# Kernel optimization log

Measured on AMD Instinct MI355X. Metric: run time of the kernel, lower is better.

## Reference

```python
import jax, jax.numpy as jnp
import numpy as np

B = 65536
IN = 64
H = 16
PF = 64


def _linear_params(key, out_dim, in_dim):
    k1, k2 = jax.random.split(key)
    bound = 1.0 / np.sqrt(in_dim)
    W = jax.random.uniform(k1, (out_dim, in_dim), jnp.float32, -bound, bound)
    b = jax.random.uniform(k2, (out_dim,), jnp.float32, -bound, bound)
    return W, b


def setup_inputs() -> dict:
    key = jax.random.key(0)
    ks = jax.random.split(key, 20)
    inp = {}
    for i, name in enumerate(['a', 'v', 'l', 'p_a', 'p_v', 'p_l', 'mean']):
        inp[name] = jax.random.normal(ks[i], (B, IN), jnp.float32)
    inp['Wa'], inp['ba'] = _linear_params(ks[7], H, IN)
    inp['Wv'], inp['bv'] = _linear_params(ks[8], H, IN)
    inp['Wl'], inp['bl'] = _linear_params(ks[9], H, IN)
    inp['Wap'], inp['bap'] = _linear_params(ks[10], H, IN)
    inp['Wvp'], inp['bvp'] = _linear_params(ks[11], H, IN)
    inp['Wlp'], inp['blp'] = _linear_params(ks[12], H, IN)
    inp['Wf1'], inp['bf1'] = _linear_params(ks[13], PF, H ** 3 // 16)
    inp['Wfp1'], inp['bfp1'] = _linear_params(ks[14], PF, H ** 3 // 16)
    inp['Wng'], inp['bng'] = _linear_params(ks[15], 64, 128)
    inp['rm1'] = jnp.zeros((128,), jnp.float32)  # normGate2 running_mean buffers (eval mode)
    inp['rm2'] = jnp.zeros((128,), jnp.float32)
    return inp


def _maxpool2(x):
    # 2x2 stride-2 max pool over the last two dims of [B, Hd, Wd]
    b, hd, wd = x.shape
    return x.reshape(b, hd // 2, 2, wd // 2, 2).max(axis=(2, 4))


def _trimodal_fusion(x_h, y_h, z_h):
    # outer product [B,H,H] -> pool -> [B,H*H//4,1] bmm [B,1,H] -> pool -> flatten
    f = x_h[:, :, None] * y_h[:, None, :]            # [B,16,16]
    f = _maxpool2(f)                                 # [B,8,8]
    f = f.reshape(-1, H * H // 4, 1) * z_h[:, None, :]  # [B,64,16]
    f = _maxpool2(f)                                 # [B,32,8]
    return f.reshape(x_h.shape[0], -1)               # [B,256]


def _norm_gate(x, running_mean):
    # eval-mode normGate2: y = x * sigmoid(|x - running_mean|)
    return x * jax.nn.sigmoid(jnp.abs(x - running_mean))


def reference(a, v, l, p_a, p_v, p_l, mean,
              Wa, ba, Wv, bv, Wl, bl, Wap, bap, Wvp, bvp, Wlp, blp,
              Wf1, bf1, Wfp1, bfp1, Wng, bng, rm1, rm2):
    a_h = jax.nn.sigmoid(a @ Wa.T + ba)
    v_h = jax.nn.sigmoid(v @ Wv.T + bv)
    l_h = jax.nn.sigmoid(l @ Wl.T + bl)
    fusion_1 = jax.nn.leaky_relu(_trimodal_fusion(a_h, v_h, l_h) @ Wf1.T + bf1)

    pa_h = jax.nn.sigmoid(p_a @ Wap.T + bap)
    pv_h = jax.nn.sigmoid(p_v @ Wvp.T + bvp)
    pl_h = jax.nn.sigmoid(p_l @ Wlp.T + blp)
    fusion_2 = jax.nn.leaky_relu(_trimodal_fusion(pa_h, pv_h, pl_h) @ Wfp1.T + bfp1)

    out = _norm_gate(jnp.concatenate([fusion_2, mean], axis=1), rm1)   # [B,128]
    out = out @ Wng.T + bng                                            # [B,64]
    out = _norm_gate(jnp.concatenate([out, fusion_1], axis=1), rm2)    # [B,128]
    return out
```

## Files before the change

kernel.cpp:

```cpp
#include <hip/hip_runtime.h>
#include <hip/hip_bf16.h>


typedef __attribute__((ext_vector_type(8))) short short8;
typedef __attribute__((ext_vector_type(4))) float f32x4;

#define MFMA16(A, B, C) __builtin_amdgcn_mfma_f32_16x16x32_bf16((A), (B), (C), 0, 0, 0)

__device__ __forceinline__ float fast_sigmoid(float x) {
    return __builtin_amdgcn_rcpf(1.0f + __expf(-x));
}
__device__ __forceinline__ float gate(float x, float rm) {
    return x * fast_sigmoid(fabsf(x - rm));
}
__device__ __forceinline__ float lrelu(float x) {
    return x >= 0.0f ? x : 0.01f * x;
}
__device__ __forceinline__ short f2bf(float f) {
    union { float f; unsigned u; } x; x.f = f;
    unsigned r = (x.u + 0x7FFF + ((x.u >> 16) & 1)) >> 16;
    return (short)r;
}
__device__ __forceinline__ short8 pack8(const float* xs) {
    union { short8 s; __hip_bfloat162 h[4]; } u;
    #pragma unroll
    for (int i = 0; i < 4; ++i) {
        float2 t; t.x = xs[2 * i]; t.y = xs[2 * i + 1];
        u.h[i] = __float22bfloat162_rn(t);
    }
    return u.s;
}
__device__ __forceinline__ f32x4 pmax_xor(f32x4 v, int mask) {
    f32x4 r;
    #pragma unroll
    for (int i = 0; i < 4; ++i) r[i] = fmaxf(v[i], __shfl_xor(v[i], mask, 64));
    return r;
}

__device__ __forceinline__ void dma_1k(const short* src, short* dst_lds, int lane) {
    __builtin_amdgcn_global_load_lds(
        (const __attribute__((address_space(1))) unsigned int*)(const void*)(src + lane * 8),
        (__attribute__((address_space(3))) unsigned int*)(void*)(dst_lds),
        16, 0, 0);
}

__device__ __forceinline__ void proj_mfma2r(const float4* in,
                                            const short8* __restrict__ wfr,
                                            const float* __restrict__ bias,
                                            int lane, f32x4& h0, f32x4& h1) {
    const int m = lane & 15;
    f32x4 a0; a0[0] = a0[1] = a0[2] = a0[3] = 0.0f;
    f32x4 a1 = a0;
    #pragma unroll
    for (int t = 0; t < 2; ++t) {
        const short8 frag = wfr[t * 64 + lane];
        float xs0[8] = {in[2*t].x, in[2*t].y, in[2*t].z, in[2*t].w,
                        in[2*t+1].x, in[2*t+1].y, in[2*t+1].z, in[2*t+1].w};
        float xs1[8] = {in[4+2*t].x, in[4+2*t].y, in[4+2*t].z, in[4+2*t].w,
                        in[4+2*t+1].x, in[4+2*t+1].y, in[4+2*t+1].z, in[4+2*t+1].w};
        a0 = MFMA16(pack8(xs0), frag, a0);
        a1 = MFMA16(pack8(xs1), frag, a1);
    }
    const float bn = bias[m];
    #pragma unroll
    for (int r = 0; r < 4; ++r) {
        h0[r] = fast_sigmoid(a0[r] + bn);
        h1[r] = fast_sigmoid(a1[r] + bn);
    }
}

__device__ __forceinline__ void stage_pools(f32x4 hx, f32x4 hy, f32x4 hz, int lane,
                                            float* __restrict__ sX,
                                            float* __restrict__ sY,
                                            float* __restrict__ sZ) {
    const int quad = lane >> 4, ln = lane & 15;
    f32x4 X = pmax_xor(hx, 1);
    f32x4 Y = pmax_xor(pmax_xor(hy, 1), 2);
    f32x4 Z = pmax_xor(hz, 1);
    #pragma unroll
    for (int r = 0; r < 4; ++r) {
        const int sm = quad * 4 + r;
        sX[(ln >> 1) * 16 + sm] = X[r];
        sY[(ln >> 2) * 16 + sm] = Y[r];
        sZ[(ln >> 1) * 16 + sm] = Z[r];
    }
}

__device__ __forceinline__ void fusion_mfma2(const short8* __restrict__ wfr,
                                             const float* __restrict__ bias,
                                             const float* __restrict__ sP0,
                                             const float* __restrict__ sP1,
                                             int lane,
                                             f32x4 acc0[4], f32x4 acc1[4]) {
    const int m = lane & 15, quad = lane >> 4;
    const float* sX0 = sP0; const float* sY0 = sP0 + 128; const float* sZ0 = sP0 + 192;
    const float* sX1 = sP1; const float* sY1 = sP1 + 128; const float* sZ1 = sP1 + 192;
    #pragma unroll
    for (int nt = 0; nt < 4; ++nt) {
        const float bb = bias[nt * 16 + m];
        acc0[nt][0] = acc0[nt][1] = acc0[nt][2] = acc0[nt][3] = bb;
        acc1[nt][0] = acc1[nt][1] = acc1[nt][2] = acc1[nt][3] = bb;
    }
    float zr0[8], zr1[8], xr0[8], xr1[8];
    #pragma unroll
    for (int j = 0; j < 8; ++j) {
        zr0[j] = sZ0[j * 16 + m]; zr1[j] = sZ1[j * 16 + m];
        xr0[j] = sX0[j * 16 + m]; xr1[j] = sX1[j * 16 + m];
    }
    const float yq0 = sY0[quad * 16 + m];
    const float yq1 = sY1[quad * 16 + m];
    #pragma unroll
    for (int t = 0; t < 8; ++t) {
        const float xy0 = xr0[t] * yq0;
        const float xy1 = xr1[t] * yq1;
        float p0[8], p1[8];
        #pragma unroll
        for (int j = 0; j < 8; ++j) { p0[j] = xy0 * zr0[j]; p1[j] = xy1 * zr1[j]; }
        const short8 af0 = pack8(p0);
        const short8 af1 = pack8(p1);
        #pragma unroll
        for (int nt = 0; nt < 4; ++nt) {
            const short8 frag = wfr[(t * 4 + nt) * 64 + lane];
            acc0[nt] = MFMA16(af0, frag, acc0[nt]);
            acc1[nt] = MFMA16(af1, frag, acc1[nt]);
        }
    }
}

__global__ __launch_bounds__(256, 2)
void fused_fwd(const float* __restrict__ a,  const float* __restrict__ v,
               const float* __restrict__ l,  const float* __restrict__ pa,
               const float* __restrict__ pv, const float* __restrict__ pl,
               const float* __restrict__ mean,
               const float* __restrict__ ba,  const float* __restrict__ bv_,
               const float* __restrict__ bl_, const float* __restrict__ bap,
               const float* __restrict__ bvp, const float* __restrict__ blp,
               const float* __restrict__ bf1, const float* __restrict__ bfp1,
               const float* __restrict__ bng,
               const float* __restrict__ rm1, const float* __restrict__ rm2,
               const short* __restrict__ ws, float* __restrict__ out) {
    __shared__ __align__(16) short sFrag[27648];
    __shared__ __align__(16) float sScr[4][1280];

    const int tid = threadIdx.x;
    const int lane = tid & 63;
    const int w = tid >> 6;
    const int m = lane & 15;
    const int quad = lane >> 4;
    const int p1 = blockIdx.x & 1;
    const int p  = blockIdx.x >> 1;

    {
        const int nU = p1 ? 38 : 54;
        for (int u = w; u < nU; u += 4) {
            const short* src;
            if (u < 6)       src = ws + (p1 ? 0 : 3072) + u * 512;
            else if (u < 38) src = ws + (p1 ? 6144 : 22528) + (u - 6) * 512;
            else             src = ws + 38912 + (u - 38) * 512;
            dma_1k(src, sFrag + u * 512, lane);
        }
    }
    __syncthreads();

    const short8* projT = (const short8*)sFrag;
    const short8* fusT  = (const short8*)(sFrag + 3072);
    const short8* ngT   = (const short8*)(sFrag + 19456);

    float* sP0 = sScr[w];
    float* sP1 = sP0 + 320;
    short* sF0 = (short*)sScr[w];
    short* sF1 = sF0 + 1280;

    for (int c = 0; c < 2; ++c) {
        const int srow0 = (p * 2 + c) * 128 + w * 32;

        if (!p1) {
            float4 inA[8], inB[8], inC[8], inM[8];
            {
                const float* x0 = pa + (size_t)srow0 * 64;
                const float* x1 = pv + (size_t)srow0 * 64;
                const float* x2 = pl + (size_t)srow0 * 64;
                #pragma unroll
                for (int i = 0; i < 8; ++i) {
                    const int tile = i >> 2, t = (i >> 1) & 1, hf = i & 1;
                    const size_t off = (size_t)(tile * 16 + m) * 64 + t * 32 + quad * 8 + hf * 4;
                    inA[i] = *(const float4*)(x0 + off);
                    inB[i] = *(const float4*)(x1 + off);
                    inC[i] = *(const float4*)(x2 + off);
                    inM[i] = *(const float4*)(mean + (size_t)(srow0 + tile * 16 + m) * 64
                                              + t * 32 + quad * 8 + hf * 4);
                }
            }

            f32x4 hx0, hx1, hy0, hy1, hz0, hz1;
            proj_mfma2r(inA, projT + 0 * 128, bap, lane, hx0, hx1);
            proj_mfma2r(inB, projT + 1 * 128, bvp, lane, hy0, hy1);
            proj_mfma2r(inC, projT + 2 * 128, blp, lane, hz0, hz1);
            stage_pools(hx0, hy0, hz0, lane, sP0, sP0 + 128, sP0 + 192);
            stage_pools(hx1, hy1, hz1, lane, sP1, sP1 + 128, sP1 + 192);

            f32x4 f20[4], f21[4];
            fusion_mfma2(fusT, bfp1, sP0, sP1, lane, f20, f21);

            #pragma unroll
            for (int nt = 0; nt < 4; ++nt) {
                const float r1 = rm1[nt * 16 + m];
                #pragma unroll
                for (int r = 0; r < 4; ++r) {
                    sF0[(quad * 4 + r) * 80 + nt * 16 + m] = f2bf(gate(lrelu(f20[nt][r]), r1));
                    sF1[(quad * 4 + r) * 80 + nt * 16 + m] = f2bf(gate(lrelu(f21[nt][r]), r1));
                }
            }

            f32x4 h0[4], h1[4];
            #pragma unroll
            for (int nt = 0; nt < 4; ++nt) {
                const float bb = bng[nt * 16 + m];
                h0[nt][0] = h0[nt][1] = h0[nt][2] = h0[nt][3] = bb;
                h1[nt][0] = h1[nt][1] = h1[nt][2] = h1[nt][3] = bb;
            }
            #pragma unroll
            for (int t = 0; t < 2; ++t) {
                const short8 af0 = *(const short8*)(sF0 + m * 80 + t * 32 + quad * 8);
                const short8 af1 = *(const short8*)(sF1 + m * 80 + t * 32 + quad * 8);
                #pragma unroll
                for (int nt = 0; nt < 4; ++nt) {
                    const short8 frag = ngT[(t * 4 + nt) * 64 + lane];
                    h0[nt] = MFMA16(af0, frag, h0[nt]);
                    h1[nt] = MFMA16(af1, frag, h1[nt]);
                }
            }
            #pragma unroll
            for (int t2 = 0; t2 < 2; ++t2) {
                const float4* rp = (const float4*)(rm1 + 64 + t2 * 32 + quad * 8);
                float4 r0 = rp[0], r1 = rp[1];
                float4 u0 = inM[2 * t2], u1 = inM[2 * t2 + 1];
                float4 w0 = inM[4 + 2 * t2], w1 = inM[4 + 2 * t2 + 1];
                float g0[8] = { gate(u0.x, r0.x), gate(u0.y, r0.y), gate(u0.z, r0.z), gate(u0.w, r0.w),
                                gate(u1.x, r1.x), gate(u1.y, r1.y), gate(u1.z, r1.z), gate(u1.w, r1.w) };
                float g1[8] = { gate(w0.x, r0.x), gate(w0.y, r0.y), gate(w0.z, r0.z), gate(w0.w, r0.w),
                                gate(w1.x, r1.x), gate(w1.y, r1.y), gate(w1.z, r1.z), gate(w1.w, r1.w) };
                const short8 af0 = pack8(g0);
                const short8 af1 = pack8(g1);
                #pragma unroll
                for (int nt = 0; nt < 4; ++nt) {
                    const short8 frag = ngT[((2 + t2) * 4 + nt) * 64 + lane];
                    h0[nt] = MFMA16(af0, frag, h0[nt]);
                    h1[nt] = MFMA16(af1, frag, h1[nt]);
                }
            }

            #pragma unroll
            for (int nt = 0; nt < 4; ++nt) {
                const float r2a = rm2[nt * 16 + m];
                #pragma unroll
                for (int r = 0; r < 4; ++r) {
                    const size_t row0 = (size_t)(srow0 + quad * 4 + r) * 128;
                    const size_t row1 = (size_t)(srow0 + 16 + quad * 4 + r) * 128;
                    out[row0 + nt * 16 + m] = gate(h0[nt][r], r2a);
                    out[row1 + nt * 16 + m] = gate(h1[nt][r], r2a);
                }
            }
        } else {
            float4 inA[8], inB[8], inC[8];
            {
                const float* x0 = a + (size_t)srow0 * 64;
                const float* x1 = v + (size_t)srow0 * 64;
                const float* x2 = l + (size_t)srow0 * 64;
                #pragma unroll
                for (int i = 0; i < 8; ++i) {
                    const int tile = i >> 2, t = (i >> 1) & 1, hf = i & 1;
                    const size_t off = (size_t)(tile * 16 + m) * 64 + t * 32 + quad * 8 + hf * 4;
                    inA[i] = *(const float4*)(x0 + off);
                    inB[i] = *(const float4*)(x1 + off);
                    inC[i] = *(const float4*)(x2 + off);
                }
            }

            f32x4 hx0, hx1, hy0, hy1, hz0, hz1;
            proj_mfma2r(inA, projT + 0 * 128, ba, lane, hx0, hx1);
            proj_mfma2r(inB, projT + 1 * 128, bv_, lane, hy0, hy1);
            proj_mfma2r(inC, projT + 2 * 128, bl_, lane, hz0, hz1);
            stage_pools(hx0, hy0, hz0, lane, sP0, sP0 + 128, sP0 + 192);
            stage_pools(hx1, hy1, hz1, lane, sP1, sP1 + 128, sP1 + 192);

            f32x4 f10[4], f11[4];
            fusion_mfma2(fusT, bf1, sP0, sP1, lane, f10, f11);

            #pragma unroll
            for (int nt = 0; nt < 4; ++nt) {
                const float r2b = rm2[64 + nt * 16 + m];
                #pragma unroll
                for (int r = 0; r < 4; ++r) {
                    const size_t row0 = (size_t)(srow0 + quad * 4 + r) * 128;
                    const size_t row1 = (size_t)(srow0 + 16 + quad * 4 + r) * 128;
                    out[row0 + 64 + nt * 16 + m] = gate(lrelu(f10[nt][r]), r2b);
                    out[row1 + 64 + nt * 16 + m] = gate(lrelu(f11[nt][r]), r2b);
                }
            }
        }
    }
}

__global__ void build_frags(const float* __restrict__ Wa,  const float* __restrict__ Wv,
                            const float* __restrict__ Wl,  const float* __restrict__ Wap,
                            const float* __restrict__ Wvp, const float* __restrict__ Wlp,
                            const float* __restrict__ Wf1, const float* __restrict__ Wfp1,
                            const float* __restrict__ Wng, short* __restrict__ ws) {
    const int i = blockIdx.x * 256 + threadIdx.x;
    if (i >= 47104) return;
    float val;
    if (i < 6144) {
        const float* W[6] = {Wa, Wv, Wl, Wap, Wvp, Wlp};
        const int mi = i >> 10, r = i & 1023;
        const int t = r >> 9, lane = (r >> 3) & 63, j = r & 7;
        val = W[mi][(lane & 15) * 64 + t * 32 + (lane >> 4) * 8 + j];
    } else if (i < 38912) {
        int r = i - 6144;
        const float* W = (r < 16384) ? Wf1 : Wfp1;
        r &= 16383;
        const int tn = r >> 9, lane = (r >> 3) & 63, j = r & 7;
        const int t = tn >> 2, nt = tn & 3;
        val = W[(nt * 16 + (lane & 15)) * 256 + t * 32 + (lane >> 4) * 8 + j];
    } else {
        const int r = i - 38912;
        const int tn = r >> 9, lane = (r >> 3) & 63, j = r & 7;
        const int t = tn >> 2, nt = tn & 3;
        val = Wng[(nt * 16 + (lane & 15)) * 128 + t * 32 + (lane >> 4) * 8 + j];
    }
    ws[i] = f2bf(val);
}

extern "C" void kernel_launch(void* const* d_in, const int* in_sizes, int n_in,
                              void* d_out, int out_size, void* d_ws, size_t ws_size,
                              hipStream_t stream) {
    const float* a    = (const float*)d_in[0];
    const float* v    = (const float*)d_in[1];
    const float* l    = (const float*)d_in[2];
    const float* pa   = (const float*)d_in[3];
    const float* pv   = (const float*)d_in[4];
    const float* pl   = (const float*)d_in[5];
    const float* mean = (const float*)d_in[6];
    const float* Wa   = (const float*)d_in[7];
    const float* ba   = (const float*)d_in[8];
    const float* Wv   = (const float*)d_in[9];
    const float* bv   = (const float*)d_in[10];
    const float* Wl   = (const float*)d_in[11];
    const float* bl   = (const float*)d_in[12];
    const float* Wap  = (const float*)d_in[13];
    const float* bap  = (const float*)d_in[14];
    const float* Wvp  = (const float*)d_in[15];
    const float* bvp  = (const float*)d_in[16];
    const float* Wlp  = (const float*)d_in[17];
    const float* blp  = (const float*)d_in[18];
    const float* Wf1  = (const float*)d_in[19];
    const float* bf1  = (const float*)d_in[20];
    const float* Wfp1 = (const float*)d_in[21];
    const float* bfp1 = (const float*)d_in[22];
    const float* Wng  = (const float*)d_in[23];
    const float* bng  = (const float*)d_in[24];
    const float* rm1  = (const float*)d_in[25];
    const float* rm2  = (const float*)d_in[26];

    short* ws = (short*)d_ws;

    build_frags<<<184, 256, 0, stream>>>(Wa, Wv, Wl, Wap, Wvp, Wlp,
                                         Wf1, Wfp1, Wng, ws);
    fused_fwd<<<512, 256, 0, stream>>>(a, v, l, pa, pv, pl, mean,
                                       ba, bv, bl, bap, bvp, blp,
                                       bf1, bfp1, bng, rm1, rm2,
                                       ws, (float*)d_out);
}
```

Before: 42.43 us.

## Issue input loads via inline asm with staged vmcnt waits; stage biases in LDS

Input loads now go through inline-asm global_load_dwordx4, grouped per tensor. Explicit s_waitcnt vmcnt(N) barriers let each projection start as soon as its own input has arrived, instead of waiting for all loads. The mean-tensor wait is pushed back to just before its use. Biases and running means are packed into the workspace by build_frags and copied into LDS alongside the weight fragments, which removes scattered global loads from the compute path. This relies on the vmcnt counts matching the issued loads exactly, and the asm volatile loads block compiler reordering.

```diff
diff --git a/kernel.cpp b/kernel.cpp
--- a/kernel.cpp
+++ b/kernel.cpp
@@ -6,6 +6,11 @@
 typedef __attribute__((ext_vector_type(4))) float f32x4;
 
 #define MFMA16(A, B, C) __builtin_amdgcn_mfma_f32_16x16x32_bf16((A), (B), (C), 0, 0, 0)
+
+#define ASM_LOAD_F4(dst, p) \
+    asm volatile("global_load_dwordx4 %0, %1, off" : "=v"(dst) : "v"(p) : "memory")
+#define VMWAIT(N) do { asm volatile("s_waitcnt vmcnt(" #N ")" ::: "memory"); \
+                       __builtin_amdgcn_sched_barrier(0); } while (0)
 
 __device__ __forceinline__ float fast_sigmoid(float x) {
     return __builtin_amdgcn_rcpf(1.0f + __expf(-x));
@@ -44,7 +49,7 @@
         16, 0, 0);
 }
 
-__device__ __forceinline__ void proj_mfma2r(const float4* in,
+__device__ __forceinline__ void proj_mfma2r(const f32x4* in,
                                             const short8* __restrict__ wfr,
                                             const float* __restrict__ bias,
                                             int lane, f32x4& h0, f32x4& h1) {
@@ -54,10 +59,10 @@
     #pragma unroll
     for (int t = 0; t < 2; ++t) {
         const short8 frag = wfr[t * 64 + lane];
-        float xs0[8] = {in[2*t].x, in[2*t].y, in[2*t].z, in[2*t].w,
-                        in[2*t+1].x, in[2*t+1].y, in[2*t+1].z, in[2*t+1].w};
-        float xs1[8] = {in[4+2*t].x, in[4+2*t].y, in[4+2*t].z, in[4+2*t].w,
-                        in[4+2*t+1].x, in[4+2*t+1].y, in[4+2*t+1].z, in[4+2*t+1].w};
+        float xs0[8] = {in[2*t][0], in[2*t][1], in[2*t][2], in[2*t][3],
+                        in[2*t+1][0], in[2*t+1][1], in[2*t+1][2], in[2*t+1][3]};
+        float xs1[8] = {in[4+2*t][0], in[4+2*t][1], in[4+2*t][2], in[4+2*t][3],
+                        in[4+2*t+1][0], in[4+2*t+1][1], in[4+2*t+1][2], in[4+2*t+1][3]};
         a0 = MFMA16(pack8(xs0), frag, a0);
         a1 = MFMA16(pack8(xs1), frag, a1);
     }
@@ -132,15 +137,10 @@
                const float* __restrict__ l,  const float* __restrict__ pa,
                const float* __restrict__ pv, const float* __restrict__ pl,
                const float* __restrict__ mean,
-               const float* __restrict__ ba,  const float* __restrict__ bv_,
-               const float* __restrict__ bl_, const float* __restrict__ bap,
-               const float* __restrict__ bvp, const float* __restrict__ blp,
-               const float* __restrict__ bf1, const float* __restrict__ bfp1,
-               const float* __restrict__ bng,
-               const float* __restrict__ rm1, const float* __restrict__ rm2,
                const short* __restrict__ ws, float* __restrict__ out) {
     __shared__ __align__(16) short sFrag[27648];
     __shared__ __align__(16) float sScr[4][1280];
+    __shared__ __align__(16) float sBias[368];
 
     const int tid = threadIdx.x;
     const int lane = tid & 63;
@@ -159,12 +159,25 @@
             else             src = ws + 38912 + (u - 38) * 512;
             dma_1k(src, sFrag + u * 512, lane);
         }
+        const float* wsF = (const float*)(ws + 47104);
+        const int bOff = p1 ? 0 : 176;
+        const int bCnt = p1 ? 176 : 368;
+        for (int t = tid; t < bCnt; t += 256) sBias[t] = wsF[bOff + t];
     }
     __syncthreads();
 
     const short8* projT = (const short8*)sFrag;
     const short8* fusT  = (const short8*)(sFrag + 3072);
     const short8* ngT   = (const short8*)(sFrag + 19456);
+
+    const float* bA = sBias;
+    const float* bB = sBias + 16;
+    const float* bC = sBias + 32;
+    const float* bF = sBias + 48;
+    const float* bNG  = sBias + 112;
+    const float* RM1  = sBias + 176;
+    const float* RM2A = sBias + 304;
+    const float* RM2B = sBias + 112;
 
     float* sP0 = sScr[w];
     float* sP1 = sP0 + 320;
@@ -175,36 +188,54 @@
         const int srow0 = (p * 2 + c) * 128 + w * 32;
 
         if (!p1) {
-            float4 inA[8], inB[8], inC[8], inM[8];
+            f32x4 inA[8], inB[8], inC[8], inM[8];
             {
                 const float* x0 = pa + (size_t)srow0 * 64;
                 const float* x1 = pv + (size_t)srow0 * 64;
                 const float* x2 = pl + (size_t)srow0 * 64;
-                #pragma unroll
-                for (int i = 0; i < 8; ++i) {
-                    const int tile = i >> 2, t = (i >> 1) & 1, hf = i & 1;
-                    const size_t off = (size_t)(tile * 16 + m) * 64 + t * 32 + quad * 8 + hf * 4;
-                    inA[i] = *(const float4*)(x0 + off);
-                    inB[i] = *(const float4*)(x1 + off);
-                    inC[i] = *(const float4*)(x2 + off);
-                    inM[i] = *(const float4*)(mean + (size_t)(srow0 + tile * 16 + m) * 64
-                                              + t * 32 + quad * 8 + hf * 4);
+                const float* x3 = mean + (size_t)srow0 * 64;
+                #pragma unroll
+                for (int i = 0; i < 8; ++i) {
+                    const int tile = i >> 2, t = (i >> 1) & 1, hf = i & 1;
+                    const size_t off = (size_t)(tile * 16 + m) * 64 + t * 32 + quad * 8 + hf * 4;
+                    ASM_LOAD_F4(inA[i], x0 + off);
+                }
+                #pragma unroll
+                for (int i = 0; i < 8; ++i) {
+                    const int tile = i >> 2, t = (i >> 1) & 1, hf = i & 1;
+                    const size_t off = (size_t)(tile * 16 + m) * 64 + t * 32 + quad * 8 + hf * 4;
+                    ASM_LOAD_F4(inB[i], x1 + off);
+                }
+                #pragma unroll
+                for (int i = 0; i < 8; ++i) {
+                    const int tile = i >> 2, t = (i >> 1) & 1, hf = i & 1;
+                    const size_t off = (size_t)(tile * 16 + m) * 64 + t * 32 + quad * 8 + hf * 4;
+                    ASM_LOAD_F4(inC[i], x2 + off);
+                }
+                #pragma unroll
+                for (int i = 0; i < 8; ++i) {
+                    const int tile = i >> 2, t = (i >> 1) & 1, hf = i & 1;
+                    const size_t off = (size_t)(tile * 16 + m) * 64 + t * 32 + quad * 8 + hf * 4;
+                    ASM_LOAD_F4(inM[i], x3 + off);
                 }
             }
 
             f32x4 hx0, hx1, hy0, hy1, hz0, hz1;
-            proj_mfma2r(inA, projT + 0 * 128, bap, lane, hx0, hx1);
-            proj_mfma2r(inB, projT + 1 * 128, bvp, lane, hy0, hy1);
-            proj_mfma2r(inC, projT + 2 * 128, blp, lane, hz0, hz1);
+            VMWAIT(24);
+            proj_mfma2r(inA, projT + 0 * 128, bA, lane, hx0, hx1);
+            VMWAIT(16);
+            proj_mfma2r(inB, projT + 1 * 128, bB, lane, hy0, hy1);
+            VMWAIT(8);
+            proj_mfma2r(inC, projT + 2 * 128, bC, lane, hz0, hz1);
             stage_pools(hx0, hy0, hz0, lane, sP0, sP0 + 128, sP0 + 192);
             stage_pools(hx1, hy1, hz1, lane, sP1, sP1 + 128, sP1 + 192);
 
             f32x4 f20[4], f21[4];
-            fusion_mfma2(fusT, bfp1, sP0, sP1, lane, f20, f21);
+            fusion_mfma2(fusT, bF, sP0, sP1, lane, f20, f21);
 
             #pragma unroll
             for (int nt = 0; nt < 4; ++nt) {
-                const float r1 = rm1[nt * 16 + m];
+                const float r1 = RM1[nt * 16 + m];
                 #pragma unroll
                 for (int r = 0; r < 4; ++r) {
                     sF0[(quad * 4 + r) * 80 + nt * 16 + m] = f2bf(gate(lrelu(f20[nt][r]), r1));
@@ -215,7 +246,7 @@
             f32x4 h0[4], h1[4];
             #pragma unroll
             for (int nt = 0; nt < 4; ++nt) {
-                const float bb = bng[nt * 16 + m];
+                const float bb = bNG[nt * 16 + m];
                 h0[nt][0] = h0[nt][1] = h0[nt][2] = h0[nt][3] = bb;
                 h1[nt][0] = h1[nt][1] = h1[nt][2] = h1[nt][3] = bb;
             }
@@ -230,16 +261,17 @@
                     h1[nt] = MFMA16(af1, frag, h1[nt]);
                 }
             }
+            VMWAIT(0);
             #pragma unroll
             for (int t2 = 0; t2 < 2; ++t2) {
-                const float4* rp = (const float4*)(rm1 + 64 + t2 * 32 + quad * 8);
-                float4 r0 = rp[0], r1 = rp[1];
-                float4 u0 = inM[2 * t2], u1 = inM[2 * t2 + 1];
-                float4 w0 = inM[4 + 2 * t2], w1 = inM[4 + 2 * t2 + 1];
-                float g0[8] = { gate(u0.x, r0.x), gate(u0.y, r0.y), gate(u0.z, r0.z), gate(u0.w, r0.w),
-                                gate(u1.x, r1.x), gate(u1.y, r1.y), gate(u1.z, r1.z), gate(u1.w, r1.w) };
-                float g1[8] = { gate(w0.x, r0.x), gate(w0.y, r0.y), gate(w0.z, r0.z), gate(w0.w, r0.w),
-                                gate(w1.x, r1.x), gate(w1.y, r1.y), gate(w1.z, r1.z), gate(w1.w, r1.w) };
+                const f32x4 r0 = *(const f32x4*)(RM1 + 64 + t2 * 32 + quad * 8);
+                const f32x4 r1 = *(const f32x4*)(RM1 + 64 + t2 * 32 + quad * 8 + 4);
+                const f32x4 u0 = inM[2 * t2],     u1 = inM[2 * t2 + 1];
+                const f32x4 w0 = inM[4 + 2 * t2], w1 = inM[4 + 2 * t2 + 1];
+                float g0[8] = { gate(u0[0], r0[0]), gate(u0[1], r0[1]), gate(u0[2], r0[2]), gate(u0[3], r0[3]),
+                                gate(u1[0], r1[0]), gate(u1[1], r1[1]), gate(u1[2], r1[2]), gate(u1[3], r1[3]) };
+                float g1[8] = { gate(w0[0], r0[0]), gate(w0[1], r0[1]), gate(w0[2], r0[2]), gate(w0[3], r0[3]),
+                                gate(w1[0], r1[0]), gate(w1[1], r1[1]), gate(w1[2], r1[2]), gate(w1[3], r1[3]) };
                 const short8 af0 = pack8(g0);
                 const short8 af1 = pack8(g1);
                 #pragma unroll
@@ -252,7 +284,7 @@
 
             #pragma unroll
             for (int nt = 0; nt < 4; ++nt) {
-                const float r2a = rm2[nt * 16 + m];
+                const float r2a = RM2A[nt * 16 + m];
                 #pragma unroll
                 for (int r = 0; r < 4; ++r) {
                     const size_t row0 = (size_t)(srow0 + quad * 4 + r) * 128;
@@ -262,7 +294,7 @@
                 }
             }
         } else {
-            float4 inA[8], inB[8], inC[8];
+            f32x4 inA[8], inB[8], inC[8];
             {
                 const float* x0 = a + (size_t)srow0 * 64;
                 const float* x1 = v + (size_t)srow0 * 64;
@@ -271,25 +303,38 @@
                 for (int i = 0; i < 8; ++i) {
                     const int tile = i >> 2, t = (i >> 1) & 1, hf = i & 1;
                     const size_t off = (size_t)(tile * 16 + m) * 64 + t * 32 + quad * 8 + hf * 4;
-                    inA[i] = *(const float4*)(x0 + off);
-                    inB[i] = *(const float4*)(x1 + off);
-                    inC[i] = *(const float4*)(x2 + off);
+                    ASM_LOAD_F4(inA[i], x0 + off);
+                }
+                #pragma unroll
+                for (int i = 0; i < 8; ++i) {
+                    const int tile = i >> 2, t = (i >> 1) & 1, hf = i & 1;
+                    const size_t off = (size_t)(tile * 16 + m) * 64 + t * 32 + quad * 8 + hf * 4;
+                    ASM_LOAD_F4(inB[i], x1 + off);
+                }
+                #pragma unroll
+                for (int i = 0; i < 8; ++i) {
+                    const int tile = i >> 2, t = (i >> 1) & 1, hf = i & 1;
+                    const size_t off = (size_t)(tile * 16 + m) * 64 + t * 32 + quad * 8 + hf * 4;
+                    ASM_LOAD_F4(inC[i], x2 + off);
                 }
             }
 
             f32x4 hx0, hx1, hy0, hy1, hz0, hz1;
-            proj_mfma2r(inA, projT + 0 * 128, ba, lane, hx0, hx1);
-            proj_mfma2r(inB, projT + 1 * 128, bv_, lane, hy0, hy1);
-            proj_mfma2r(inC, projT + 2 * 128, bl_, lane, hz0, hz1);
+            VMWAIT(16);
+            proj_mfma2r(inA, projT + 0 * 128, bA, lane, hx0, hx1);
+            VMWAIT(8);
+            proj_mfma2r(inB, projT + 1 * 128, bB, lane, hy0, hy1);
+            VMWAIT(0);
+            proj_mfma2r(inC, projT + 2 * 128, bC, lane, hz0, hz1);
             stage_pools(hx0, hy0, hz0, lane, sP0, sP0 + 128, sP0 + 192);
             stage_pools(hx1, hy1, hz1, lane, sP1, sP1 + 128, sP1 + 192);
 
             f32x4 f10[4], f11[4];
-            fusion_mfma2(fusT, bf1, sP0, sP1, lane, f10, f11);
+            fusion_mfma2(fusT, bF, sP0, sP1, lane, f10, f11);
 
             #pragma unroll
             for (int nt = 0; nt < 4; ++nt) {
-                const float r2b = rm2[64 + nt * 16 + m];
+                const float r2b = RM2B[nt * 16 + m];
                 #pragma unroll
                 for (int r = 0; r < 4; ++r) {
                     const size_t row0 = (size_t)(srow0 + quad * 4 + r) * 128;
@@ -306,9 +351,37 @@
                             const float* __restrict__ Wl,  const float* __restrict__ Wap,
                             const float* __restrict__ Wvp, const float* __restrict__ Wlp,
                             const float* __restrict__ Wf1, const float* __restrict__ Wfp1,
-                            const float* __restrict__ Wng, short* __restrict__ ws) {
+                            const float* __restrict__ Wng,
+                            const float* __restrict__ ba,  const float* __restrict__ bv,
+                            const float* __restrict__ bl,  const float* __restrict__ bap,
+                            const float* __restrict__ bvp, const float* __restrict__ blp,
+                            const float* __restrict__ bf1, const float* __restrict__ bfp1,
+                            const float* __restrict__ bng, const float* __restrict__ rm1,
+                            const float* __restrict__ rm2, short* __restrict__ ws) {
     const int i = blockIdx.x * 256 + threadIdx.x;
-    if (i >= 47104) return;
+    if (i >= 47104 + 544) return;
+    if (i >= 47104) {
+        const int j = i - 47104;
+        float fv;
+        if (j < 176) {
+            if (j < 16)       fv = ba[j];
+            else if (j < 32)  fv = bv[j - 16];
+            else if (j < 48)  fv = bl[j - 32];
+            else if (j < 112) fv = bf1[j - 48];
+            else              fv = rm2[64 + (j - 112)];
+        } else {
+            const int k = j - 176;
+            if (k < 16)       fv = bap[k];
+            else if (k < 32)  fv = bvp[k - 16];
+            else if (k < 48)  fv = blp[k - 32];
+            else if (k < 112) fv = bfp1[k - 48];
+            else if (k < 176) fv = bng[k - 112];
+            else if (k < 304) fv = rm1[k - 176];
+            else              fv = rm2[k - 304];
+        }
+        ((float*)(ws + 47104))[j] = fv;
+        return;
+    }
     float val;
     if (i < 6144) {
         const float* W[6] = {Wa, Wv, Wl, Wap, Wvp, Wlp};
@@ -364,10 +437,10 @@
 
     short* ws = (short*)d_ws;
 
-    build_frags<<<184, 256, 0, stream>>>(Wa, Wv, Wl, Wap, Wvp, Wlp,
-                                         Wf1, Wfp1, Wng, ws);
+    build_frags<<<187, 256, 0, stream>>>(Wa, Wv, Wl, Wap, Wvp, Wlp,
+                                         Wf1, Wfp1, Wng,
+                                         ba, bv, bl, bap, bvp, blp,
+                                         bf1, bfp1, bng, rm1, rm2, ws);
     fused_fwd<<<512, 256, 0, stream>>>(a, v, l, pa, pv, pl, mean,
-                                       ba, bv, bl, bap, bvp, blp,
-                                       bf1, bfp1, bng, rm1, rm2,
                                        ws, (float*)d_out);
 }
```

New measurement: 38.41 us. -9.5%, faster.
